# Kernel optimization log

Hardware: AMD Instinct MI355X
Metric: run time of the kernel (lower is better)

Reference implementation:

```python
import jax, jax.numpy as jnp
import numpy as np

EPS = 1e-12


def _l2norm(x):
    # F.normalize(x, dim=1): x / max(||x||, eps)
    n = jnp.sqrt(jnp.sum(x * x, axis=1, keepdims=True))
    return x / jnp.maximum(n, EPS)


def _remove_diag(x):
    # x: [n, n] -> [n, n-1], dropping the diagonal (matches x[~eye].view(n, -1))
    n = x.shape[0]
    row = jnp.arange(n)[:, None]
    base = jnp.arange(n - 1)[None, :]
    cols = jnp.where(base < row, base, base + 1)  # column indices != row index
    return jnp.take_along_axis(x, cols, axis=1)


def _lid_mle(data, reference, k):
    # pairwise euclidean distances [n_data, n_ref]
    d2 = (jnp.sum(data * data, axis=1)[:, None]
          + jnp.sum(reference * reference, axis=1)[None, :]
          - 2.0 * data @ reference.T)
    dist = jnp.sqrt(jnp.maximum(d2, 0.0))
    # k+1 smallest distances (index 0 is the self-distance since data subset of reference)
    neg_top, _ = jax.lax.top_k(-dist, k + 1)
    d = -neg_top[:, 1:]  # [n, k], ascending, self excluded
    # MLE LID estimator: -k / sum_i log(d_i / d_k)
    return -k / jnp.sum(jnp.log(d / d[:, -1:] + EPS), axis=1)


def _byol_loss(p, z):
    z = jax.lax.stop_gradient(z)
    return 2.0 - 2.0 * jnp.sum(_l2norm(p) * _l2norm(z), axis=1)


def _track_logits(o0, o1):
    b = o0.shape[0]
    l00 = _remove_diag(jnp.einsum('nc,mc->nm', o0, o0))
    l01 = jnp.einsum('nc,mc->nm', o0, o1)
    l10 = jnp.einsum('nc,mc->nm', o1, o0)
    l11 = _remove_diag(jnp.einsum('nc,mc->nm', o1, o1))
    logits = jnp.concatenate([
        jnp.concatenate([l01, l00], axis=1),
        jnp.concatenate([l10, l11], axis=1)], axis=0)  # [2b, 2b-1]
    labels = jnp.tile(jnp.arange(b, dtype=jnp.int32), 2)
    return logits, labels


def setup_inputs() -> dict:
    key = jax.random.key(0)
    ks = jax.random.split(key, 9)
    B, Dfe, Dp, C = 4096, 2048, 256, 1000
    return {
        'fe_0': jax.random.normal(ks[0], (B, Dfe), jnp.float32),
        'fe_1': jax.random.normal(ks[1], (B, Dfe), jnp.float32),
        'p_0': jax.random.normal(ks[2], (B, Dp), jnp.float32),
        'p_1': jax.random.normal(ks[3], (B, Dp), jnp.float32),
        'z_0': jax.random.normal(ks[4], (B, Dp), jnp.float32),
        'z_1': jax.random.normal(ks[5], (B, Dp), jnp.float32),
        'cls_0': jax.random.normal(ks[6], (B, C), jnp.float32),
        'cls_1': jax.random.normal(ks[7], (B, C), jnp.float32),
        'online_labels': jax.random.randint(ks[8], (B,), 0, C, jnp.int32),
    }


def reference(fe_0, fe_1, p_0, p_1, z_0, z_1, cls_0, cls_1, online_labels):
    # BYOL symmetric loss
    main_loss = jnp.mean(_byol_loss(p_0, z_1) + _byol_loss(p_1, z_0))
    # online linear-probe cross-entropy on concatenated views
    cls = jnp.concatenate([cls_0, cls_1], axis=0)
    labels2 = jnp.concatenate([online_labels, online_labels], axis=0)
    logp = jax.nn.log_softmax(cls, axis=1)
    online_loss = -jnp.mean(jnp.take_along_axis(logp, labels2[:, None], axis=1)[:, 0])
    # LID tracking on backbone features (no-grad in original)
    fe = jnp.concatenate([fe_0, fe_1], axis=0)
    lids32 = _lid_mle(fe, fe, 32)
    lids512 = _lid_mle(fe, fe, 512)
    # contrastive-style logit tracking on normalized predictor outputs
    logits, labels = _track_logits(_l2norm(p_0), _l2norm(p_1))
    return main_loss, online_loss, logits, labels, lids32, lids512
```

## Files before the change

### kernel.cpp

```cpp
#include <hip/hip_runtime.h>
#include <math.h>

typedef __bf16 bf16;
typedef __bf16 bf16x8 __attribute__((ext_vector_type(8)));
typedef __bf16 bf16x4 __attribute__((ext_vector_type(4)));
typedef float f32x4 __attribute__((ext_vector_type(4)));

#define NROW 8192
#define BHALF 4096
#define DFE 2048
#define DP 256
#define NCLS 1000

#define LOGITS_N 8191
#define OUT_LOGITS 2
#define OUT_LABELS (2 + 8192 * 8191)
#define OUT_LIDS32 (OUT_LABELS + 8192)
#define OUT_LIDS512 (OUT_LIDS32 + 8192)

#define G0TILES 528
#define G1TILES 1024

__device__ inline void gload16(const bf16* g, bf16* l) {
    __builtin_amdgcn_global_load_lds((const __attribute__((address_space(1))) void*)g,
                                     (__attribute__((address_space(3))) void*)l, 16, 0, 0);
}

__global__ __launch_bounds__(256) void init_kernel(float* out) {
    int i = blockIdx.x * 256 + threadIdx.x;
    if (i < 2) out[i] = 0.f;
    if (i < NROW) out[(size_t)OUT_LABELS + i] = (float)(i & (BHALF - 1));
}

__global__ __launch_bounds__(256) void split_fe_kernel(const float* __restrict__ fe0,
                                                       const float* __restrict__ fe1,
                                                       bf16* __restrict__ feh,
                                                       bf16* __restrict__ fel,
                                                       float* __restrict__ norms) {
    int row = blockIdx.x, tid = threadIdx.x;
    const float* src = (row < BHALF) ? fe0 + (size_t)row * DFE
                                     : fe1 + (size_t)(row - BHALF) * DFE;
    float ss = 0.f;
#pragma unroll
    for (int pass = 0; pass < 2; ++pass) {
        int c = (pass * 256 + tid) * 4;
        float4 v = *(const float4*)(src + c);
        ss += v.x * v.x + v.y * v.y + v.z * v.z + v.w * v.w;
        bf16 h0 = (bf16)v.x, h1 = (bf16)v.y, h2 = (bf16)v.z, h3 = (bf16)v.w;
        bf16 l0 = (bf16)(v.x - (float)h0), l1 = (bf16)(v.y - (float)h1);
        bf16 l2 = (bf16)(v.z - (float)h2), l3 = (bf16)(v.w - (float)h3);
        bf16x4 hv = {h0, h1, h2, h3};
        bf16x4 lv = {l0, l1, l2, l3};
        *(bf16x4*)(feh + (size_t)row * DFE + c) = hv;
        *(bf16x4*)(fel + (size_t)row * DFE + c) = lv;
    }
#pragma unroll
    for (int off = 32; off; off >>= 1) ss += __shfl_down(ss, off);
    __shared__ float red[4];
    if ((tid & 63) == 0) red[tid >> 6] = ss;
    __syncthreads();
    if (tid == 0) norms[row] = red[0] + red[1] + red[2] + red[3];
}

__global__ __launch_bounds__(256) void norm_split_p_kernel(const float* __restrict__ p0,
                                                           const float* __restrict__ p1,
                                                           bf16* __restrict__ oh) {
    int row = blockIdx.x, tid = threadIdx.x;
    const float* src = (row < BHALF) ? p0 + (size_t)row * DP
                                     : p1 + (size_t)(row - BHALF) * DP;
    float x = src[tid];
    float ss = x * x;
#pragma unroll
    for (int off = 32; off; off >>= 1) ss += __shfl_down(ss, off);
    __shared__ float red[4];
    if ((tid & 63) == 0) red[tid >> 6] = ss;
    __syncthreads();
    float tot = red[0] + red[1] + red[2] + red[3];
    float rn = 1.f / fmaxf(sqrtf(tot), 1e-12f);
    oh[(size_t)row * DP + tid] = (bf16)(x * rn);
}

__device__ inline float dot4(float4 a, float4 b) {
    return a.x * b.x + a.y * b.y + a.z * b.z + a.w * b.w;
}

__global__ __launch_bounds__(256) void byol_kernel(const float* __restrict__ p0,
                                                   const float* __restrict__ p1,
                                                   const float* __restrict__ z0,
                                                   const float* __restrict__ z1,
                                                   float* out) {
    int tid = threadIdx.x, wave = tid >> 6, lane = tid & 63;
    int row = blockIdx.x * 4 + wave;
    size_t base = (size_t)row * DP + lane * 4;
    float4 a0 = *(const float4*)(p0 + base);
    float4 b0 = *(const float4*)(z1 + base);
    float4 a1 = *(const float4*)(p1 + base);
    float4 b1 = *(const float4*)(z0 + base);
    float pp0 = dot4(a0, a0), zz0 = dot4(b0, b0), pz0 = dot4(a0, b0);
    float pp1 = dot4(a1, a1), zz1 = dot4(b1, b1), pz1 = dot4(a1, b1);
#pragma unroll
    for (int off = 32; off; off >>= 1) {
        pp0 += __shfl_down(pp0, off); zz0 += __shfl_down(zz0, off); pz0 += __shfl_down(pz0, off);
        pp1 += __shfl_down(pp1, off); zz1 += __shfl_down(zz1, off); pz1 += __shfl_down(pz1, off);
    }
    __shared__ float red[4];
    if (lane == 0) {
        float c0 = pz0 / (fmaxf(sqrtf(pp0), 1e-12f) * fmaxf(sqrtf(zz0), 1e-12f));
        float c1 = pz1 / (fmaxf(sqrtf(pp1), 1e-12f) * fmaxf(sqrtf(zz1), 1e-12f));
        red[wave] = (2.f - 2.f * c0) + (2.f - 2.f * c1);
    }
    __syncthreads();
    if (tid == 0) atomicAdd(out, (red[0] + red[1] + red[2] + red[3]) * (1.f / 4096.f));
}

__global__ __launch_bounds__(256) void online_kernel(const float* __restrict__ cls0,
                                                     const float* __restrict__ cls1,
                                                     const int* __restrict__ labels,
                                                     float* out) {
    int tid = threadIdx.x, wave = tid >> 6, lane = tid & 63;
    int row = blockIdx.x * 4 + wave;
    const float* src = (row < BHALF) ? cls0 + (size_t)row * NCLS
                                     : cls1 + (size_t)(row - BHALF) * NCLS;
    int lbl = labels[row & (BHALF - 1)];
    float xs[16];
    float mx = -INFINITY;
#pragma unroll
    for (int j = 0; j < 16; ++j) {
        int c = lane + j * 64;
        xs[j] = (c < NCLS) ? src[c] : -INFINITY;
        mx = fmaxf(mx, xs[j]);
    }
#pragma unroll
    for (int off = 32; off; off >>= 1) mx = fmaxf(mx, __shfl_xor(mx, off));
    float se = 0.f;
#pragma unroll
    for (int j = 0; j < 16; ++j) se += expf(xs[j] - mx);
#pragma unroll
    for (int off = 32; off; off >>= 1) se += __shfl_xor(se, off);
    __shared__ float red[4];
    if (lane == 0) red[wave] = src[lbl] - mx - logf(se);
    __syncthreads();
    if (tid == 0) atomicAdd(out + 1, -(red[0] + red[1] + red[2] + red[3]) * (1.f / 8192.f));
}

__global__ __launch_bounds__(512, 2) void gemm_kernel(const bf16* __restrict__ Hp,
                                                      const bf16* __restrict__ Lp,
                                                      const bf16* __restrict__ OHp,
                                                      const float* __restrict__ norms,
                                                      float* __restrict__ d2,
                                                      float* __restrict__ outlog) {
    __shared__ bf16 sm[2][32768];
    int tid = threadIdx.x, lane = tid & 63, wave = tid >> 6;
    int wr = wave >> 2, wn = wave & 3;
    int lrow = lane & 15, lquad = lane >> 4, r7 = lrow & 7, pg = lquad ^ r7;
    int rsub = lane >> 3, grp = lane & 7, lg = grp ^ rsub;

    int bid = blockIdx.x;
    int mode, tm, tn, ksh;
    const bf16 *Hmat, *Lmat;
    int Kd;
    if (bid < G0TILES) {
        mode = 0;
        int sw = (bid & 7) * (G0TILES / 8) + (bid >> 3);
        int i = 0;
        while ((i + 1) * (64 - i) / 2 <= sw) ++i;
        tm = i;
        tn = tm + (sw - i * (65 - i) / 2);
        Hmat = Hp; Lmat = Lp; Kd = DFE; ksh = 5;
    } else {
        mode = 1;
        int id = bid - G0TILES;
        int sw = (id & 7) * (G1TILES / 8) + (id >> 3);
        tm = sw & 31; tn = sw >> 5;
        Hmat = OHp; Lmat = OHp; Kd = DP; ksh = 2;
    }
    int NT = (mode == 0 ? 3 : 1) << ksh;
    int kmask = (1 << ksh) - 1;
    int arow0 = tm * 256, brow0 = tn * 256;
    size_t delta = (size_t)(Lmat - Hmat);

    const bf16* baseA0 = Hmat + (size_t)(arow0 + wave * 8 + rsub) * Kd + lg * 8;
    const bf16* baseB0 = Hmat + (size_t)(brow0 + wave * 8 + rsub) * Kd + lg * 8;

    int aoffbase[2], boffbase[2];
    aoffbase[0] = (wr * 64 + lrow) * 128 + pg * 16;
    aoffbase[1] = aoffbase[0] + 128 * 128;
    boffbase[0] = 32768 + (wn * 32 + lrow) * 128 + pg * 16;
    boffbase[1] = boffbase[0] + 128 * 128;

    f32x4 acc[8][4];
    f32x4 zz = {0.f, 0.f, 0.f, 0.f};
#pragma unroll
    for (int i = 0; i < 8; ++i)
#pragma unroll
        for (int j = 0; j < 4; ++j) acc[i][j] = zz;

#define STAGE_A(tau, h, dstbuf)                                                   \
    do {                                                                          \
        int tau_ = (tau);                                                         \
        if (tau_ < NT) {                                                          \
            int ch_ = tau_ >> ksh;                                                \
            size_t dd_ = (ch_ == 1) ? delta : 0;                                  \
            int k_ = (tau_ & kmask) << 6;                                         \
            bf16* d_ = (dstbuf) + (h) * 8192 + wave * 512;                        \
            gload16(baseA0 + (size_t)((h) * 128) * Kd + dd_ + k_, d_);            \
            gload16(baseA0 + (size_t)((h) * 128 + 64) * Kd + dd_ + k_, d_ + 4096);\
        }                                                                         \
    } while (0)

#define STAGE_B(tau, h, dstbuf)                                                   \
    do {                                                                          \
        int tau_ = (tau);                                                         \
        if (tau_ < NT) {                                                          \
            int ch_ = tau_ >> ksh;                                                \
            size_t dd_ = (ch_ == 2) ? delta : 0;                                  \
            int k_ = (tau_ & kmask) << 6;                                         \
            bf16* d_ = (dstbuf) + 16384 + (h) * 8192 + wave * 512;                \
            gload16(baseB0 + (size_t)((h) * 128) * Kd + dd_ + k_, d_);            \
            gload16(baseB0 + (size_t)((h) * 128 + 64) * Kd + dd_ + k_, d_ + 4096);\
        }                                                                         \
    } while (0)

#define READ_A(AF, MI)                                                            \
    do {                                                                          \
        _Pragma("unroll") for (int f = 0; f < 4; ++f) {                           \
            int off_ = aoffbase[(MI)] + f * 2048;                                 \
            AF[f][0] = *(const bf16x8*)(Sb + off_);                               \
            AF[f][1] = *(const bf16x8*)(Sb + (off_ ^ 64));                        \
        }                                                                         \
    } while (0)

#define READ_B(BF, NI)                                                            \
    do {                                                                          \
        _Pragma("unroll") for (int jj = 0; jj < 2; ++jj) {                        \
            int off_ = boffbase[(NI)] + jj * 2048;                                \
            BF[jj][0] = *(const bf16x8*)(Sb + off_);                              \
            BF[jj][1] = *(const bf16x8*)(Sb + (off_ ^ 64));                       \
        }                                                                         \
    } while (0)

#define MFMA_PHASE(MI, NI, AF, BF)                                                \
    do {                                                                          \
        __builtin_amdgcn_s_setprio(1);                                            \
        _Pragma("unroll") for (int f = 0; f < 4; ++f)                             \
            _Pragma("unroll") for (int jj = 0; jj < 2; ++jj) {                    \
                acc[(MI)*4 + f][(NI)*2 + jj] = __builtin_amdgcn_mfma_f32_16x16x32_bf16( \
                    AF[f][0], BF[jj][0], acc[(MI)*4 + f][(NI)*2 + jj], 0, 0, 0);  \
                acc[(MI)*4 + f][(NI)*2 + jj] = __builtin_amdgcn_mfma_f32_16x16x32_bf16( \
                    AF[f][1], BF[jj][1], acc[(MI)*4 + f][(NI)*2 + jj], 0, 0, 0);  \
            }                                                                     \
        __builtin_amdgcn_s_setprio(0);                                            \
    } while (0)

#define VM_END(tailflag)                                                          \
    do {                                                                          \
        if (tailflag) asm volatile("s_waitcnt vmcnt(0)" ::: "memory");            \
        else          asm volatile("s_waitcnt vmcnt(10)" ::: "memory");           \
    } while (0)

    bf16x8 af[4][2], b0f[2][2], b1f[2][2];

    STAGE_A(0, 0, sm[0]); STAGE_B(0, 0, sm[0]); STAGE_B(0, 1, sm[0]); STAGE_A(0, 1, sm[0]);
    STAGE_A(1, 0, sm[1]); STAGE_B(1, 0, sm[1]); STAGE_B(1, 1, sm[1]);
    asm volatile("s_waitcnt vmcnt(10)" ::: "memory");
    __builtin_amdgcn_s_barrier();

    for (int t = 0; t < NT; ++t) {
        const char* Sb = (const char*)sm[t & 1];
        bf16* samebuf = sm[t & 1];
        bf16* otherbuf = sm[(t + 1) & 1];
        bool tail = (t >= NT - 3);

        READ_A(af, 0);
        READ_B(b0f, 0);
        STAGE_A(t + 1, 1, otherbuf);
        __builtin_amdgcn_s_barrier();
        asm volatile("s_waitcnt lgkmcnt(0)" ::: "memory");
        __builtin_amdgcn_sched_barrier(0);
        MFMA_PHASE(0, 0, af, b0f);
        VM_END(tail);
        __builtin_amdgcn_s_barrier();

        READ_B(b1f, 1);
        STAGE_A(t + 2, 0, samebuf);
        __builtin_amdgcn_s_barrier();
        asm volatile("s_waitcnt lgkmcnt(0)" ::: "memory");
        __builtin_amdgcn_sched_barrier(0);
        MFMA_PHASE(0, 1, af, b1f);
        VM_END(tail);
        __builtin_amdgcn_s_barrier();

        READ_A(af, 1);
        STAGE_B(t + 2, 0, samebuf);
        __builtin_amdgcn_s_barrier();
        asm volatile("s_waitcnt lgkmcnt(0)" ::: "memory");
        __builtin_amdgcn_sched_barrier(0);
        MFMA_PHASE(1, 0, af, b0f);
        if (tail) asm volatile("s_waitcnt vmcnt(0)" ::: "memory");
        __builtin_amdgcn_s_barrier();

        STAGE_B(t + 2, 1, samebuf);
        __builtin_amdgcn_s_barrier();
        __builtin_amdgcn_sched_barrier(0);
        MFMA_PHASE(1, 1, af, b1f);
        VM_END(tail);
        __builtin_amdgcn_s_barrier();
    }

    if (mode == 0) {
#pragma unroll
        for (int i = 0; i < 8; ++i) {
#pragma unroll
            for (int e = 0; e < 4; ++e) {
                int grow = arow0 + (i >> 2) * 128 + wr * 64 + (i & 3) * 16 + lquad * 4 + e;
                float na = norms[grow];
#pragma unroll
                for (int j = 0; j < 4; ++j) {
                    int gcol = brow0 + (j >> 1) * 128 + wn * 32 + (j & 1) * 16 + lrow;
                    float v = na + norms[gcol] - 2.f * acc[i][j][e];
                    d2[(size_t)grow * NROW + gcol] = fmaxf(v, 0.f);
                }
            }
        }
    } else {
#pragma unroll
        for (int i = 0; i < 8; ++i) {
#pragma unroll
            for (int j = 0; j < 4; ++j) {
#pragma unroll
                for (int e = 0; e < 4; ++e) {
                    int r = arow0 + (i >> 2) * 128 + wr * 64 + (i & 3) * 16 + lquad * 4 + e;
                    int c = brow0 + (j >> 1) * 128 + wn * 32 + (j & 1) * 16 + lrow;
                    int oc = 0;
                    bool skip = false;
                    if (r < BHALF) {
                        if (c >= BHALF) oc = c - BHALF;
                        else if (c == r) skip = true;
                        else oc = BHALF + (c < r ? c : c - 1);
                    } else {
                        int rp = r - BHALF;
                        if (c < BHALF) oc = c;
                        else {
                            int cp = c - BHALF;
                            if (cp == rp) skip = true;
                            else oc = BHALF + (cp < rp ? cp : cp - 1);
                        }
                    }
                    if (!skip) outlog[(size_t)r * LOGITS_N + oc] = acc[i][j][e];
                }
            }
        }
    }
#undef STAGE_A
#undef STAGE_B
#undef READ_A
#undef READ_B
#undef MFMA_PHASE
#undef VM_END
}

__global__ __launch_bounds__(256) void mirror_kernel(float* __restrict__ d2) {
    int bj = blockIdx.x, bi = blockIdx.y;
    if (bi < bj) return;
    __shared__ float t[64][65];
    int tx = threadIdx.x & 63, ty = threadIdx.x >> 6;
#pragma unroll
    for (int r = 0; r < 64; r += 4)
        t[r + ty][tx] = d2[(size_t)(bj * 64 + r + ty) * NROW + bi * 64 + tx];
    __syncthreads();
#pragma unroll
    for (int r = 0; r < 64; r += 4) {
        int gi = bi * 64 + r + ty, gj = bj * 64 + tx;
        if (gi > gj) d2[(size_t)gi * NROW + gj] = t[tx][r + ty];
    }
}

__global__ __launch_bounds__(256) void select_kernel(const float* __restrict__ d2,
                                                     float* __restrict__ out) {
    int wave = threadIdx.x >> 6, lane = threadIdx.x & 63;
    int row = blockIdx.x * 4 + wave;
    const float4* drow4 = (const float4*)(d2 + (size_t)row * NROW);
    unsigned v[128];
    unsigned andv = 0xFFFFFFFFu, orv = 0u;
#pragma unroll
    for (int j = 0; j < 32; ++j) {
        int idx4 = j * 64 + lane;
        float4 f = drow4[idx4];
        int c0 = idx4 * 4;
        unsigned u0 = __float_as_uint(f.x), u1 = __float_as_uint(f.y);
        unsigned u2 = __float_as_uint(f.z), u3 = __float_as_uint(f.w);
        bool s0 = (c0 == row), s1 = (c0 + 1 == row), s2 = (c0 + 2 == row), s3 = (c0 + 3 == row);
        v[j * 4 + 0] = s0 ? 0xFFFFFFFFu : u0;
        v[j * 4 + 1] = s1 ? 0xFFFFFFFFu : u1;
        v[j * 4 + 2] = s2 ? 0xFFFFFFFFu : u2;
        v[j * 4 + 3] = s3 ? 0xFFFFFFFFu : u3;
        andv &= (s0 ? 0xFFFFFFFFu : u0); orv |= (s0 ? 0u : u0);
        andv &= (s1 ? 0xFFFFFFFFu : u1); orv |= (s1 ? 0u : u1);
        andv &= (s2 ? 0xFFFFFFFFu : u2); orv |= (s2 ? 0u : u2);
        andv &= (s3 ? 0xFFFFFFFFu : u3); orv |= (s3 ? 0u : u3);
    }
#pragma unroll
    for (int off = 32; off; off >>= 1) {
        andv &= __shfl_xor(andv, off);
        orv |= __shfl_xor(orv, off);
    }
    unsigned diff = andv ^ orv;
    int msb = 31 - __clz((int)(diff | 1u));
    unsigned common = (msb == 31) ? 0u : (andv & (0xFFFFFFFFu << (msb + 1)));
    unsigned p1 = common, p2 = common;
    for (int bit = msb; bit >= 0; --bit) {
        unsigned c1 = p1 | (1u << bit), c2 = p2 | (1u << bit);
        unsigned n1 = 0, n2 = 0;
#pragma unroll
        for (int j = 0; j < 128; ++j) { n1 += (v[j] < c1); n2 += (v[j] < c2); }
#pragma unroll
        for (int off = 32; off; off >>= 1) {
            n1 += __shfl_xor(n1, off);
            n2 += __shfl_xor(n2, off);
        }
        if (n1 < 32u) p1 = c1;
        if (n2 < 512u) p2 = c2;
    }
    float dk1 = sqrtf(__uint_as_float(p1));
    float dk2 = sqrtf(__uint_as_float(p2));
    float s1 = 0.f, s2 = 0.f;
#pragma unroll
    for (int j = 0; j < 128; ++j) {
        unsigned b = v[j];
        if (b < p2) {
            float d = sqrtf(__uint_as_float(b));
            s2 += logf(d / dk2 + 1e-12f);
            if (b < p1) s1 += logf(d / dk1 + 1e-12f);
        }
    }
#pragma unroll
    for (int off = 32; off; off >>= 1) {
        s1 += __shfl_xor(s1, off);
        s2 += __shfl_xor(s2, off);
    }
    if (lane == 0) {
        out[(size_t)OUT_LIDS32 + row] = -32.f / s1;
        out[(size_t)OUT_LIDS512 + row] = -512.f / s2;
    }
}

extern "C" void kernel_launch(void* const* d_in, const int* in_sizes, int n_in,
                              void* d_out, int out_size, void* d_ws, size_t ws_size,
                              hipStream_t stream) {
    const float* fe0 = (const float*)d_in[0];
    const float* fe1 = (const float*)d_in[1];
    const float* p0 = (const float*)d_in[2];
    const float* p1 = (const float*)d_in[3];
    const float* z0 = (const float*)d_in[4];
    const float* z1 = (const float*)d_in[5];
    const float* cls0 = (const float*)d_in[6];
    const float* cls1 = (const float*)d_in[7];
    const int* labels = (const int*)d_in[8];
    float* out = (float*)d_out;

    char* ws = (char*)d_ws;
    float* D2 = (float*)ws;
    bf16* FEH = (bf16*)(ws + 268435456UL);
    bf16* FEL = (bf16*)(ws + 268435456UL + 33554432UL);
    bf16* OH = (bf16*)(ws + 268435456UL + 2 * 33554432UL);
    float* NORMS = (float*)(ws + 268435456UL + 2 * 33554432UL + 4194304UL);

    init_kernel<<<32, 256, 0, stream>>>(out);
    split_fe_kernel<<<8192, 256, 0, stream>>>(fe0, fe1, FEH, FEL, NORMS);
    norm_split_p_kernel<<<8192, 256, 0, stream>>>(p0, p1, OH);
    byol_kernel<<<1024, 256, 0, stream>>>(p0, p1, z0, z1, out);
    online_kernel<<<2048, 256, 0, stream>>>(cls0, cls1, labels, out);
    gemm_kernel<<<G0TILES + G1TILES, 512, 0, stream>>>(FEH, FEL, OH, NORMS, D2, out + OUT_LOGITS);
    mirror_kernel<<<dim3(128, 128), 256, 0, stream>>>(D2);
    select_kernel<<<2048, 256, 0, stream>>>(D2, out);
}
```

Before: 1.292 ms.

## Restructure GEMM main loop to two barriers with register double-buffered fragments

```diff
diff --git a/kernel.cpp b/kernel.cpp
--- a/kernel.cpp
+++ b/kernel.cpp
@@ -195,47 +195,40 @@
 #pragma unroll
         for (int j = 0; j < 4; ++j) acc[i][j] = zz;
 
-#define STAGE_A(tau, h, dstbuf)                                                   \
+#define STAGE_ALL(tau, dstbuf)                                                    \
     do {                                                                          \
         int tau_ = (tau);                                                         \
         if (tau_ < NT) {                                                          \
             int ch_ = tau_ >> ksh;                                                \
-            size_t dd_ = (ch_ == 1) ? delta : 0;                                  \
+            size_t dA_ = (ch_ == 1) ? delta : 0;                                  \
+            size_t dB_ = (ch_ == 2) ? delta : 0;                                  \
             int k_ = (tau_ & kmask) << 6;                                         \
-            bf16* d_ = (dstbuf) + (h) * 8192 + wave * 512;                        \
-            gload16(baseA0 + (size_t)((h) * 128) * Kd + dd_ + k_, d_);            \
-            gload16(baseA0 + (size_t)((h) * 128 + 64) * Kd + dd_ + k_, d_ + 4096);\
+            bf16* da_ = (dstbuf) + wave * 512;                                    \
+            bf16* db_ = (dstbuf) + 16384 + wave * 512;                            \
+            _Pragma("unroll") for (int h = 0; h < 2; ++h) {                       \
+                gload16(baseA0 + (size_t)(h * 128) * Kd + dA_ + k_, da_ + h * 8192);          \
+                gload16(baseA0 + (size_t)(h * 128 + 64) * Kd + dA_ + k_, da_ + h * 8192 + 4096); \
+                gload16(baseB0 + (size_t)(h * 128) * Kd + dB_ + k_, db_ + h * 8192);          \
+                gload16(baseB0 + (size_t)(h * 128 + 64) * Kd + dB_ + k_, db_ + h * 8192 + 4096); \
+            }                                                                     \
         }                                                                         \
     } while (0)
 
-#define STAGE_B(tau, h, dstbuf)                                                   \
-    do {                                                                          \
-        int tau_ = (tau);                                                         \
-        if (tau_ < NT) {                                                          \
-            int ch_ = tau_ >> ksh;                                                \
-            size_t dd_ = (ch_ == 2) ? delta : 0;                                  \
-            int k_ = (tau_ & kmask) << 6;                                         \
-            bf16* d_ = (dstbuf) + 16384 + (h) * 8192 + wave * 512;                \
-            gload16(baseB0 + (size_t)((h) * 128) * Kd + dd_ + k_, d_);            \
-            gload16(baseB0 + (size_t)((h) * 128 + 64) * Kd + dd_ + k_, d_ + 4096);\
-        }                                                                         \
-    } while (0)
-
-#define READ_A(AF, MI)                                                            \
+#define READ_A(AF, MI, SB)                                                        \
     do {                                                                          \
         _Pragma("unroll") for (int f = 0; f < 4; ++f) {                           \
             int off_ = aoffbase[(MI)] + f * 2048;                                 \
-            AF[f][0] = *(const bf16x8*)(Sb + off_);                               \
-            AF[f][1] = *(const bf16x8*)(Sb + (off_ ^ 64));                        \
+            AF[f][0] = *(const bf16x8*)((SB) + off_);                             \
+            AF[f][1] = *(const bf16x8*)((SB) + (off_ ^ 64));                      \
         }                                                                         \
     } while (0)
 
-#define READ_B(BF, NI)                                                            \
+#define READ_B(BF, NI, SB)                                                        \
     do {                                                                          \
         _Pragma("unroll") for (int jj = 0; jj < 2; ++jj) {                        \
             int off_ = boffbase[(NI)] + jj * 2048;                                \
-            BF[jj][0] = *(const bf16x8*)(Sb + off_);                              \
-            BF[jj][1] = *(const bf16x8*)(Sb + (off_ ^ 64));                       \
+            BF[jj][0] = *(const bf16x8*)((SB) + off_);                            \
+            BF[jj][1] = *(const bf16x8*)((SB) + (off_ ^ 64));                     \
         }                                                                         \
     } while (0)
 
@@ -252,59 +245,50 @@
         __builtin_amdgcn_s_setprio(0);                                            \
     } while (0)
 
-#define VM_END(tailflag)                                                          \
-    do {                                                                          \
-        if (tailflag) asm volatile("s_waitcnt vmcnt(0)" ::: "memory");            \
-        else          asm volatile("s_waitcnt vmcnt(10)" ::: "memory");           \
-    } while (0)
-
-    bf16x8 af[4][2], b0f[2][2], b1f[2][2];
-
-    STAGE_A(0, 0, sm[0]); STAGE_B(0, 0, sm[0]); STAGE_B(0, 1, sm[0]); STAGE_A(0, 1, sm[0]);
-    STAGE_A(1, 0, sm[1]); STAGE_B(1, 0, sm[1]); STAGE_B(1, 1, sm[1]);
-    asm volatile("s_waitcnt vmcnt(10)" ::: "memory");
+    bf16x8 af[4][2];
+    bf16x8 af2[4][2];
+    bf16x8 b0f[2][2];
+    bf16x8 b1f[2][2];
+    const char* S0 = (const char*)sm[0];
+    const char* S1 = (const char*)sm[1];
+
+    STAGE_ALL(0, sm[0]);
+    STAGE_ALL(1, sm[1]);
+    asm volatile("s_waitcnt vmcnt(8)" ::: "memory");
     __builtin_amdgcn_s_barrier();
+    READ_A(af, 0, S0);
+    READ_B(b0f, 0, S0);
 
     for (int t = 0; t < NT; ++t) {
-        const char* Sb = (const char*)sm[t & 1];
-        bf16* samebuf = sm[t & 1];
-        bf16* otherbuf = sm[(t + 1) & 1];
-        bool tail = (t >= NT - 3);
-
-        READ_A(af, 0);
-        READ_B(b0f, 0);
-        STAGE_A(t + 1, 1, otherbuf);
+        const char* Sb = (t & 1) ? S1 : S0;
+        const char* Sbn = (t & 1) ? S0 : S1;
+        bf16* ownbuf = sm[t & 1];
+
+        READ_B(b1f, 1, Sb);
+        asm volatile("s_waitcnt lgkmcnt(4)" ::: "memory");
+        __builtin_amdgcn_sched_barrier(0);
+        MFMA_PHASE(0, 0, af, b0f);
+
+        READ_A(af2, 1, Sb);
+        asm volatile("s_waitcnt lgkmcnt(8)" ::: "memory");
+        __builtin_amdgcn_sched_barrier(0);
+        MFMA_PHASE(0, 1, af, b1f);
         __builtin_amdgcn_s_barrier();
+
         asm volatile("s_waitcnt lgkmcnt(0)" ::: "memory");
         __builtin_amdgcn_sched_barrier(0);
-        MFMA_PHASE(0, 0, af, b0f);
-        VM_END(tail);
+        STAGE_ALL(t + 2, ownbuf);
+        MFMA_PHASE(1, 0, af2, b0f);
+        if (t + 2 < NT) asm volatile("s_waitcnt vmcnt(8)" ::: "memory");
+        else            asm volatile("s_waitcnt vmcnt(0)" ::: "memory");
         __builtin_amdgcn_s_barrier();
 
-        READ_B(b1f, 1);
-        STAGE_A(t + 2, 0, samebuf);
-        __builtin_amdgcn_s_barrier();
-        asm volatile("s_waitcnt lgkmcnt(0)" ::: "memory");
+        if (t + 1 < NT) {
+            READ_A(af, 0, Sbn);
+            READ_B(b0f, 0, Sbn);
+        }
         __builtin_amdgcn_sched_barrier(0);
-        MFMA_PHASE(0, 1, af, b1f);
-        VM_END(tail);
-        __builtin_amdgcn_s_barrier();
-
-        READ_A(af, 1);
-        STAGE_B(t + 2, 0, samebuf);
-        __builtin_amdgcn_s_barrier();
-        asm volatile("s_waitcnt lgkmcnt(0)" ::: "memory");
-        __builtin_amdgcn_sched_barrier(0);
-        MFMA_PHASE(1, 0, af, b0f);
-        if (tail) asm volatile("s_waitcnt vmcnt(0)" ::: "memory");
-        __builtin_amdgcn_s_barrier();
-
-        STAGE_B(t + 2, 1, samebuf);
-        __builtin_amdgcn_s_barrier();
-        __builtin_amdgcn_sched_barrier(0);
-        MFMA_PHASE(1, 1, af, b1f);
-        VM_END(tail);
-        __builtin_amdgcn_s_barrier();
+        MFMA_PHASE(1, 1, af2, b1f);
     }
 
     if (mode == 0) {
@@ -351,12 +335,10 @@
             }
         }
     }
-#undef STAGE_A
-#undef STAGE_B
+#undef STAGE_ALL
 #undef READ_A
 #undef READ_B
 #undef MFMA_PHASE
-#undef VM_END
 }
 
 __global__ __launch_bounds__(256) void mirror_kernel(float* __restrict__ d2) {
```

Result: faster. 1.251 ms (-3.2%).
